# Kernel tuning notes

Hardware: AMD Instinct MI355X
Metric: run time of the kernel (lower is better)

The kernel has to match this reference:

```python
import jax, jax.numpy as jnp
import numpy as np

UNITS = 1024
ORDER = 256
THETA = 512.0
D_IN = 256
BATCH = 64
SEQ = 512


def _legendre_zoh(order, theta):
    """Legendre delay system (Voelker & Eliasmith 2018), ZOH-discretized at dt=1.
    Returns AT = (A_d - I).T and BT = B_d.T, matching LMUCell's stored weights."""
    Q = np.arange(order, dtype=np.float64)
    R = (2.0 * Q + 1.0)[:, None] / theta
    j, i = np.meshgrid(Q, Q)
    A = np.where(i < j, -1.0, (-1.0) ** (i - j + 1)) * R
    B = ((-1.0) ** Q)[:, None] * R
    Aj = jnp.asarray(A, jnp.float32)
    Bj = jnp.asarray(B, jnp.float32)
    Ad = jax.scipy.linalg.expm(Aj)                      # expm(A*dt), dt=1
    Bd = jnp.linalg.solve(Aj, (Ad - jnp.eye(order, dtype=jnp.float32)) @ Bj)
    AT = (Ad - jnp.eye(order, dtype=jnp.float32)).T     # (order, order)
    BT = Bd.T                                           # (1, order)
    return AT, BT


def setup_inputs() -> dict:
    key = jax.random.key(0)
    ks = jax.random.split(key, 6)
    inputs = jax.random.normal(ks[0], (BATCH, SEQ, D_IN), jnp.float32)

    def lecun_uniform(k, fan_in, shape):
        lim = np.sqrt(3.0 / fan_in).astype(np.float32)
        return jax.random.uniform(k, shape, jnp.float32, -lim, lim)

    def glorot_normal(k, fi, fo):
        std = np.sqrt(2.0 / (fi + fo)).astype(np.float32)
        return jax.random.normal(k, (fi, fo), jnp.float32) * std

    input_encoders = lecun_uniform(ks[1], D_IN, (D_IN, 1))
    hidden_encoders = lecun_uniform(ks[2], UNITS, (UNITS, 1))
    memory_encoders = jnp.zeros((ORDER, 1), jnp.float32)  # Constant(0) initializer
    input_kernel = glorot_normal(ks[3], D_IN, UNITS)
    hidden_kernel = glorot_normal(ks[4], UNITS, UNITS)
    memory_kernel = glorot_normal(ks[5], ORDER, UNITS)
    AT, BT = _legendre_zoh(ORDER, THETA)
    return {
        "inputs": inputs,
        "input_encoders": input_encoders,
        "hidden_encoders": hidden_encoders,
        "memory_encoders": memory_encoders,
        "input_kernel": input_kernel,
        "hidden_kernel": hidden_kernel,
        "memory_kernel": memory_kernel,
        "AT": AT,
        "BT": BT,
    }


def reference(inputs, input_encoders, hidden_encoders, memory_encoders,
              input_kernel, hidden_kernel, memory_kernel, AT, BT):
    B = inputs.shape[0]
    order = AT.shape[0]
    units = hidden_kernel.shape[0]
    h0 = jnp.zeros((B, units), inputs.dtype)
    m0 = jnp.zeros((B, order), inputs.dtype)

    def step(carry, x_t):
        h, m = carry
        # u: scalar encoding per batch element, shape [B, 1]
        u = x_t @ input_encoders + h @ hidden_encoders + m @ memory_encoders
        # state-space memory update: m_{t+1} = m + m @ (Ad - I)^T + u @ Bd^T
        m = m + m @ AT + u @ BT
        # hidden update (include_bias=False -> '+ 0')
        h = jnp.tanh(x_t @ input_kernel + h @ hidden_kernel + m @ memory_kernel)
        return (h, m), h

    xs = jnp.swapaxes(inputs, 0, 1)  # [T, B, D]
    (_, _), hs = jax.lax.scan(step, (h0, m0), xs)
    return jnp.swapaxes(hs, 0, 1)    # [B, T, units]
```

## Files before the change

### kernel.cpp

```cpp
#include <hip/hip_runtime.h>
#include <cmath>

static constexpr int UNITS = 1024;
static constexpr int ORDER = 256;
static constexpr int D_IN  = 256;
static constexpr int BATCH = 64;
static constexpr int SEQ   = 512;

static constexpr int GPLANE = 40960;
static constexpr int GSET   = 81920;

static constexpr size_t XE_OFF = 0;
static constexpr size_t FG_OFF = 131072;
static constexpr size_t UP_OFF = 135168;
static constexpr size_t P_OFF  = 176128;
static constexpr size_t PSET   = 327680;

static constexpr int SXH_OFF  = 0;
static constexpr int SXL_OFF  = 8448;
static constexpr int RED_OFF  = 16896;
static constexpr int RED2_OFF = 20992;
static constexpr int ULDS_OFF = 25088;
static constexpr int BVS_OFF  = 25152;
static constexpr int LDS_BYTES = 25216;

typedef __attribute__((ext_vector_type(8))) short bf16x8;
typedef __attribute__((ext_vector_type(4))) float f32x4;
typedef unsigned long long u64;

__device__ __forceinline__ unsigned short bf16rn(float f) {
    unsigned u = __builtin_bit_cast(unsigned, f);
    u += 0x7FFFu + ((u >> 16) & 1u);
    return (unsigned short)(u >> 16);
}
__device__ __forceinline__ float bf2f(unsigned short h) {
    unsigned u = ((unsigned)h) << 16;
    return __builtin_bit_cast(float, u);
}

__device__ __forceinline__ u64 ld_sys(const void* p) {
    return __hip_atomic_load((const u64*)p, __ATOMIC_RELAXED, __HIP_MEMORY_SCOPE_SYSTEM);
}
__device__ __forceinline__ void st_sys32(void* p, unsigned v) {
    __hip_atomic_store((unsigned*)p, v, __ATOMIC_RELAXED, __HIP_MEMORY_SCOPE_SYSTEM);
}
__device__ __forceinline__ bf16x8 mk8(u64 a, u64 b) {
    union { u64 q[2]; bf16x8 v; } u;
    u.q[0] = a; u.q[1] = b;
    return u.v;
}

__global__ __launch_bounds__(256) void lmu_pre(const float* __restrict__ x,
                                               const float* __restrict__ ie,
                                               char* __restrict__ ws) {
    int gid  = blockIdx.x * blockDim.x + threadIdx.x;
    int wave = gid >> 6;
    int lane = gid & 63;
    if (wave < BATCH * SEQ) {
        const float* row = x + (size_t)wave * D_IN;
        float s = 0.f;
        #pragma unroll
        for (int c = 0; c < D_IN; c += 64) s += row[c + lane] * ie[c + lane];
        #pragma unroll
        for (int off = 32; off > 0; off >>= 1) s += __shfl_down(s, off);
        if (lane == 0) ((float*)(ws + XE_OFF))[wave] = s;
    }
    if (gid < 175104) ((unsigned*)(ws + FG_OFF))[gid] = 0u;
}

__global__ __launch_bounds__(256, 1) void lmu_main(
        const float* __restrict__ x,
        const float* __restrict__ he,
        const float* __restrict__ me,
        const float* __restrict__ Wi,
        const float* __restrict__ Wh,
        const float* __restrict__ Wm,
        const float* __restrict__ AT,
        const float* __restrict__ BT,
        float* __restrict__ out,
        char* __restrict__ ws) {
    extern __shared__ char smem[];
    char*  sXH  = smem + SXH_OFF;
    char*  sXL  = smem + SXL_OFF;
    float* REDs = (float*)(smem + RED_OFF);
    float* RED2 = (float*)(smem + RED2_OFF);
    float* ULDS = (float*)(smem + ULDS_OFF);
    float* BVs  = (float*)(smem + BVS_OFF);
    float* WMC  = (float*)smem;

    const int wg = blockIdx.x, tid = threadIdx.x;
    const int wave = tid >> 6, lane = tid & 63;
    const int lrow = lane & 15, lgrp = lane >> 4;
    const int grp = wg >> 6, lid = wg & 63;
    const int b0 = grp * 16, n0 = lid * 16, nglob = n0 + lrow;
    const bool mwg = (lid < 16);
    const int mt = lid & 15;

    float* XE  = (float*)(ws + XE_OFF);
    unsigned* gf = (unsigned*)(ws + FG_OFF) + (size_t)grp * 256;
    float* UPf = (float*)(ws + UP_OFF);
    char* PB   = ws + P_OFF;

    const int lb = (lgrp * 16 + lrow) * 16;

    const int rowME = lgrp * 4 + wave;
    const int kH = 256 + n0 + (lrow & ~1);
    const int hswz = (kH / 32 - 8) * 1024 + (((kH % 32) / 8) * 16 + rowME) * 16
                   + (kH % 8) * 2;
    const int kM = 1280 + mt * 16 + (lrow & ~1);
    const int mswz = (kM / 32 - 8) * 1024 + (((kM % 32) / 8) * 16 + rowME) * 16
                   + (kM % 8) * 2;

    for (int idx = tid; idx < ORDER * 16; idx += 256)
        WMC[idx] = Wm[(size_t)(idx >> 4) * UNITS + n0 + (idx & 15)];
    __syncthreads();

    bf16x8 wfhi[12], wflo[12];
    #pragma unroll
    for (int j = 0; j < 12; ++j) {
        const int kbase = wave * 384 + j * 32 + lgrp * 8;
        bf16x8 vh, vl;
        #pragma unroll
        for (int e = 0; e < 8; ++e) {
            const int k = kbase + e;
            float f;
            if (k < 256)       f = Wi[(size_t)k * UNITS + nglob];
            else if (k < 1280) f = Wh[(size_t)(k - 256) * UNITS + nglob];
            else {
                const int r = k - 1280;
                float s = WMC[r * 16 + lrow];
                const float* atr = AT + (size_t)r * ORDER;
                for (int l = 0; l < ORDER; ++l) s += atr[l] * WMC[l * 16 + lrow];
                f = s;
            }
            unsigned short hb = bf16rn(f);
            unsigned short lb2 = bf16rn(f - bf2f(hb));
            vh[e] = (short)hb; vl[e] = (short)lb2;
        }
        wfhi[j] = vh; wflo[j] = vl;
    }
    {
        const int nl = tid & 15, seg = tid >> 4;
        float s = 0.f;
        for (int l = seg * 16; l < seg * 16 + 16; ++l) s += BT[l] * WMC[l * 16 + nl];
        REDs[tid] = s;
    }
    __syncthreads();
    if (tid < 16) {
        float s = 0.f;
        for (int sg = 0; sg < 16; ++sg) s += REDs[sg * 16 + tid];
        BVs[tid] = s;
    }
    bf16x8 m1hi[2], m1lo[2];
    float btreg = 0.f, mereg = 0.f;
    if (mwg) {
        #pragma unroll
        for (int j2 = 0; j2 < 2; ++j2) {
            const int kb = wave * 64 + j2 * 32 + lgrp * 8;
            const int c = mt * 16 + lrow;
            bf16x8 vh, vl;
            #pragma unroll
            for (int e = 0; e < 8; ++e) {
                const int r = kb + e;
                float f = AT[(size_t)r * ORDER + c] + ((r == c) ? 1.f : 0.f);
                unsigned short hb = bf16rn(f);
                unsigned short lb2 = bf16rn(f - bf2f(hb));
                vh[e] = (short)hb; vl[e] = (short)lb2;
            }
            m1hi[j2] = vh; m1lo[j2] = vl;
        }
        btreg = BT[mt * 16 + lrow];
        mereg = me[mt * 16 + lrow];
    }
    __syncthreads();
    const float bvreg = BVs[lrow];
    const float hereg = he[n0 + lrow];

    for (int t = 0; t < SEQ; ++t) {
        __syncthreads();
        if (tid == 0) {
            asm volatile("s_waitcnt vmcnt(0)\n\t"
                         "global_store_dword %0, %1, off sc0 sc1"
                         :: "v"(gf + lid), "v"((unsigned)(t + 1)) : "memory");
        }

        {
            const int row = tid >> 4, cs = tid & 15;
            const float4* xr = (const float4*)(x + ((size_t)(b0 + row) * SEQ + t) * D_IN
                                               + cs * 16);
            float4 v0 = xr[0], v1 = xr[1], v2 = xr[2], v3 = xr[3];
            float fs[16] = {v0.x,v0.y,v0.z,v0.w, v1.x,v1.y,v1.z,v1.w,
                            v2.x,v2.y,v2.z,v2.w, v3.x,v3.y,v3.z,v3.w};
            unsigned* dh = (unsigned*)(sXH + row * 528 + cs * 32);
            unsigned* dl = (unsigned*)(sXL + row * 528 + cs * 32);
            #pragma unroll
            for (int q = 0; q < 8; ++q) {
                unsigned short h0 = bf16rn(fs[2*q]),   h1 = bf16rn(fs[2*q+1]);
                unsigned short l0 = bf16rn(fs[2*q]   - bf2f(h0));
                unsigned short l1 = bf16rn(fs[2*q+1] - bf2f(h1));
                dh[q] = (unsigned)h0 | ((unsigned)h1 << 16);
                dl[q] = (unsigned)l0 | ((unsigned)l1 << 16);
            }
        }

        if (tid < 64) {
            const unsigned* fp = gf + tid;
            unsigned v;
            const unsigned gen = (unsigned)(t + 1);
            for (;;) {
                asm volatile("global_load_dword %0, %1, off sc0 sc1\n\t"
                             "s_waitcnt vmcnt(0)"
                             : "=v"(v) : "v"(fp) : "memory");
                if (v >= gen) break;
                __builtin_amdgcn_s_sleep(1);
            }
        }
        __syncthreads();
        __builtin_amdgcn_sched_barrier(0);

        const char* GH = PB + (size_t)(t & 1) * PSET + (size_t)grp * GSET;
        const char* GL = GH + GPLANE;

        u64 ah0[12], ah1[12], al0[12], al1[12];
        if (wave == 0) {
            #pragma unroll
            for (int j = 8; j < 12; ++j) {
                const int off = (j - 8) * 1024 + lb;
                ah0[j] = ld_sys(GH + off);     ah1[j] = ld_sys(GH + off + 8);
                al0[j] = ld_sys(GL + off);     al1[j] = ld_sys(GL + off + 8);
            }
        } else {
            #pragma unroll
            for (int j = 0; j < 12; ++j) {
                const int off = (wave * 12 + j - 8) * 1024 + lb;
                ah0[j] = ld_sys(GH + off);     ah1[j] = ld_sys(GH + off + 8);
                al0[j] = ld_sys(GL + off);     al1[j] = ld_sys(GL + off + 8);
            }
        }
        u64 mh0[2], mh1[2], ml0[2], ml1[2];
        if (mwg) {
            #pragma unroll
            for (int j2 = 0; j2 < 2; ++j2) {
                const int off = (32 + 2 * wave + j2) * 1024 + lb;
                mh0[j2] = ld_sys(GH + off);    mh1[j2] = ld_sys(GH + off + 8);
                ml0[j2] = ld_sys(GL + off);    ml1[j2] = ld_sys(GL + off + 8);
            }
        }
        u64 upv[10];
        if (wave == 0) {
            const int bl = lane >> 2, q = lane & 3;
            const char* pp = (const char*)(UPf + ((size_t)(t & 1) * 64 + b0 + bl) * 80
                                           + q * 20);
            #pragma unroll
            for (int i = 0; i < 10; ++i) upv[i] = ld_sys(pp + i * 8);
        }

        f32x4 acc = {0.f, 0.f, 0.f, 0.f};
        if (wave == 0) {
            #pragma unroll
            for (int j = 0; j < 8; ++j) {
                const char* xp = sXH + lrow * 528 + (j * 32 + lgrp * 8) * 2;
                bf16x8 ah = *(const bf16x8*)xp;
                bf16x8 al = *(const bf16x8*)(xp + 8448);
                acc = __builtin_amdgcn_mfma_f32_16x16x32_bf16(ah, wfhi[j], acc, 0, 0, 0);
                acc = __builtin_amdgcn_mfma_f32_16x16x32_bf16(ah, wflo[j], acc, 0, 0, 0);
                acc = __builtin_amdgcn_mfma_f32_16x16x32_bf16(al, wfhi[j], acc, 0, 0, 0);
            }
            #pragma unroll
            for (int j = 8; j < 12; ++j) {
                bf16x8 ah = mk8(ah0[j], ah1[j]);
                bf16x8 al = mk8(al0[j], al1[j]);
                acc = __builtin_amdgcn_mfma_f32_16x16x32_bf16(ah, wfhi[j], acc, 0, 0, 0);
                acc = __builtin_amdgcn_mfma_f32_16x16x32_bf16(ah, wflo[j], acc, 0, 0, 0);
                acc = __builtin_amdgcn_mfma_f32_16x16x32_bf16(al, wfhi[j], acc, 0, 0, 0);
            }
        } else {
            #pragma unroll
            for (int j = 0; j < 12; ++j) {
                bf16x8 ah = mk8(ah0[j], ah1[j]);
                bf16x8 al = mk8(al0[j], al1[j]);
                acc = __builtin_amdgcn_mfma_f32_16x16x32_bf16(ah, wfhi[j], acc, 0, 0, 0);
                acc = __builtin_amdgcn_mfma_f32_16x16x32_bf16(ah, wflo[j], acc, 0, 0, 0);
                acc = __builtin_amdgcn_mfma_f32_16x16x32_bf16(al, wfhi[j], acc, 0, 0, 0);
            }
        }
        f32x4 acc2 = {0.f, 0.f, 0.f, 0.f};
        if (mwg) {
            #pragma unroll
            for (int j2 = 0; j2 < 2; ++j2) {
                bf16x8 ah = mk8(mh0[j2], mh1[j2]);
                bf16x8 al = mk8(ml0[j2], ml1[j2]);
                acc2 = __builtin_amdgcn_mfma_f32_16x16x32_bf16(ah, m1hi[j2], acc2, 0, 0, 0);
                acc2 = __builtin_amdgcn_mfma_f32_16x16x32_bf16(ah, m1lo[j2], acc2, 0, 0, 0);
                acc2 = __builtin_amdgcn_mfma_f32_16x16x32_bf16(al, m1hi[j2], acc2, 0, 0, 0);
            }
        }

        if (wave == 0) {
            const int bl = lane >> 2, q = lane & 3;
            float s = 0.f;
            #pragma unroll
            for (int i = 0; i < 10; ++i) {
                s += __builtin_bit_cast(float, (unsigned)(upv[i] & 0xFFFFFFFFu))
                   + __builtin_bit_cast(float, (unsigned)(upv[i] >> 32));
            }
            s += __shfl_xor(s, 1, 64);
            s += __shfl_xor(s, 2, 64);
            if (q == 0) ULDS[bl] = XE[(size_t)(b0 + bl) * SEQ + t] + s;
        }

        #pragma unroll
        for (int r = 0; r < 4; ++r) {
            REDs[r * 256 + wave * 64 + lane] = acc[r];
            if (mwg) RED2[r * 256 + wave * 64 + lane] = acc2[r];
        }
        __syncthreads();

        {
            const int w = wave;
            const int b = b0 + rowME;
            float a0 = REDs[w * 256 + 0 * 64 + lane] + REDs[w * 256 + 1 * 64 + lane]
                     + REDs[w * 256 + 2 * 64 + lane] + REDs[w * 256 + 3 * 64 + lane];
            const float uu = ULDS[rowME];
            const float hval = tanhf(a0 + uu * bvreg);
            out[((size_t)b * SEQ + t) * UNITS + n0 + lrow] = hval;

            char* PNH = PB + (size_t)((t + 1) & 1) * PSET + (size_t)grp * GSET;
            char* PNL = PNH + GPLANE;
            unsigned hb = bf16rn(hval);
            unsigned lb2 = bf16rn(hval - bf2f((unsigned short)hb));
            unsigned hbn = __shfl_xor(hb, 1, 64);
            unsigned lbn = __shfl_xor(lb2, 1, 64);
            if (!(lrow & 1)) {
                st_sys32(PNH + hswz, hb | (hbn << 16));
                st_sys32(PNL + hswz, lb2 | (lbn << 16));
            }
            float ps = hval * hereg;
            ps += __shfl_xor(ps, 1, 64);
            ps += __shfl_xor(ps, 2, 64);
            ps += __shfl_xor(ps, 4, 64);
            ps += __shfl_xor(ps, 8, 64);
            float* UPn = UPf + (size_t)(((t + 1) & 1) * 64) * 80;
            if (lrow == 0)
                st_sys32(&UPn[(size_t)b * 80 + lid], __builtin_bit_cast(unsigned, ps));
            if (mwg) {
                float a2 = RED2[w * 256 + 0 * 64 + lane] + RED2[w * 256 + 1 * 64 + lane]
                         + RED2[w * 256 + 2 * 64 + lane] + RED2[w * 256 + 3 * 64 + lane];
                const float mval = a2 + uu * btreg;
                unsigned mh = bf16rn(mval);
                unsigned ml = bf16rn(mval - bf2f((unsigned short)mh));
                unsigned mhn = __shfl_xor(mh, 1, 64);
                unsigned mln = __shfl_xor(ml, 1, 64);
                if (!(lrow & 1)) {
                    st_sys32(PNH + mswz, mh | (mhn << 16));
                    st_sys32(PNL + mswz, ml | (mln << 16));
                }
                float pm = mval * mereg;
                pm += __shfl_xor(pm, 1, 64);
                pm += __shfl_xor(pm, 2, 64);
                pm += __shfl_xor(pm, 4, 64);
                pm += __shfl_xor(pm, 8, 64);
                if (lrow == 0)
                    st_sys32(&UPn[(size_t)b * 80 + 64 + mt],
                             __builtin_bit_cast(unsigned, pm));
            }
        }
    }
}

extern "C" void kernel_launch(void* const* d_in, const int* in_sizes, int n_in,
                              void* d_out, int out_size, void* d_ws, size_t ws_size,
                              hipStream_t stream) {
    const float* x  = (const float*)d_in[0];
    const float* ie = (const float*)d_in[1];
    const float* he = (const float*)d_in[2];
    const float* me = (const float*)d_in[3];
    const float* Wi = (const float*)d_in[4];
    const float* Wh = (const float*)d_in[5];
    const float* Wm = (const float*)d_in[6];
    const float* AT = (const float*)d_in[7];
    const float* BT = (const float*)d_in[8];
    float* out = (float*)d_out;
    char* ws   = (char*)d_ws;
    (void)in_sizes; (void)n_in; (void)out_size; (void)ws_size;

    hipLaunchKernelGGL(lmu_pre, dim3((BATCH * SEQ * 64) / 256), dim3(256), 0, stream,
                       x, ie, ws);

    hipLaunchKernelGGL(lmu_main, dim3(256), dim3(256), LDS_BYTES, stream,
                       x, he, me, Wi, Wh, Wm, AT, BT, out, ws);
}
```

Measured before the change: 3.070 ms.

## Balance K split across waves and use per-wave flags for grid barrier

```diff
diff --git a/kernel.cpp b/kernel.cpp
--- a/kernel.cpp
+++ b/kernel.cpp
@@ -118,7 +118,8 @@
     bf16x8 wfhi[12], wflo[12];
     #pragma unroll
     for (int j = 0; j < 12; ++j) {
-        const int kbase = wave * 384 + j * 32 + lgrp * 8;
+        const int cell = (j < 2) ? (2 * wave + j) : (8 + wave * 10 + (j - 2));
+        const int kbase = cell * 32 + lgrp * 8;
         bf16x8 vh, vl;
         #pragma unroll
         for (int e = 0; e < 8; ++e) {
@@ -177,13 +178,6 @@
     const float hereg = he[n0 + lrow];
 
     for (int t = 0; t < SEQ; ++t) {
-        __syncthreads();
-        if (tid == 0) {
-            asm volatile("s_waitcnt vmcnt(0)\n\t"
-                         "global_store_dword %0, %1, off sc0 sc1"
-                         :: "v"(gf + lid), "v"((unsigned)(t + 1)) : "memory");
-        }
-
         {
             const int row = tid >> 4, cs = tid & 15;
             const float4* xr = (const float4*)(x + ((size_t)(b0 + row) * SEQ + t) * D_IN
@@ -203,17 +197,15 @@
             }
         }
 
-        if (tid < 64) {
+        {
+            const unsigned gen = (unsigned)t;
             const unsigned* fp = gf + tid;
             unsigned v;
-            const unsigned gen = (unsigned)(t + 1);
-            for (;;) {
+            do {
                 asm volatile("global_load_dword %0, %1, off sc0 sc1\n\t"
                              "s_waitcnt vmcnt(0)"
                              : "=v"(v) : "v"(fp) : "memory");
-                if (v >= gen) break;
-                __builtin_amdgcn_s_sleep(1);
-            }
+            } while (v < gen);
         }
         __syncthreads();
         __builtin_amdgcn_sched_barrier(0);
@@ -221,21 +213,12 @@
         const char* GH = PB + (size_t)(t & 1) * PSET + (size_t)grp * GSET;
         const char* GL = GH + GPLANE;
 
-        u64 ah0[12], ah1[12], al0[12], al1[12];
-        if (wave == 0) {
-            #pragma unroll
-            for (int j = 8; j < 12; ++j) {
-                const int off = (j - 8) * 1024 + lb;
-                ah0[j] = ld_sys(GH + off);     ah1[j] = ld_sys(GH + off + 8);
-                al0[j] = ld_sys(GL + off);     al1[j] = ld_sys(GL + off + 8);
-            }
-        } else {
-            #pragma unroll
-            for (int j = 0; j < 12; ++j) {
-                const int off = (wave * 12 + j - 8) * 1024 + lb;
-                ah0[j] = ld_sys(GH + off);     ah1[j] = ld_sys(GH + off + 8);
-                al0[j] = ld_sys(GL + off);     al1[j] = ld_sys(GL + off + 8);
-            }
+        u64 ah0[10], ah1[10], al0[10], al1[10];
+        #pragma unroll
+        for (int j2 = 0; j2 < 10; ++j2) {
+            const int off = (wave * 10 + j2) * 1024 + lb;
+            ah0[j2] = ld_sys(GH + off);    ah1[j2] = ld_sys(GH + off + 8);
+            al0[j2] = ld_sys(GL + off);    al1[j2] = ld_sys(GL + off + 8);
         }
         u64 mh0[2], mh1[2], ml0[2], ml1[2];
         if (mwg) {
@@ -256,33 +239,22 @@
         }
 
         f32x4 acc = {0.f, 0.f, 0.f, 0.f};
-        if (wave == 0) {
-            #pragma unroll
-            for (int j = 0; j < 8; ++j) {
-                const char* xp = sXH + lrow * 528 + (j * 32 + lgrp * 8) * 2;
-                bf16x8 ah = *(const bf16x8*)xp;
-                bf16x8 al = *(const bf16x8*)(xp + 8448);
-                acc = __builtin_amdgcn_mfma_f32_16x16x32_bf16(ah, wfhi[j], acc, 0, 0, 0);
-                acc = __builtin_amdgcn_mfma_f32_16x16x32_bf16(ah, wflo[j], acc, 0, 0, 0);
-                acc = __builtin_amdgcn_mfma_f32_16x16x32_bf16(al, wfhi[j], acc, 0, 0, 0);
-            }
-            #pragma unroll
-            for (int j = 8; j < 12; ++j) {
-                bf16x8 ah = mk8(ah0[j], ah1[j]);
-                bf16x8 al = mk8(al0[j], al1[j]);
-                acc = __builtin_amdgcn_mfma_f32_16x16x32_bf16(ah, wfhi[j], acc, 0, 0, 0);
-                acc = __builtin_amdgcn_mfma_f32_16x16x32_bf16(ah, wflo[j], acc, 0, 0, 0);
-                acc = __builtin_amdgcn_mfma_f32_16x16x32_bf16(al, wfhi[j], acc, 0, 0, 0);
-            }
-        } else {
-            #pragma unroll
-            for (int j = 0; j < 12; ++j) {
-                bf16x8 ah = mk8(ah0[j], ah1[j]);
-                bf16x8 al = mk8(al0[j], al1[j]);
-                acc = __builtin_amdgcn_mfma_f32_16x16x32_bf16(ah, wfhi[j], acc, 0, 0, 0);
-                acc = __builtin_amdgcn_mfma_f32_16x16x32_bf16(ah, wflo[j], acc, 0, 0, 0);
-                acc = __builtin_amdgcn_mfma_f32_16x16x32_bf16(al, wfhi[j], acc, 0, 0, 0);
-            }
+        #pragma unroll
+        for (int j = 0; j < 2; ++j) {
+            const char* xp = sXH + lrow * 528 + ((2 * wave + j) * 32 + lgrp * 8) * 2;
+            bf16x8 ah = *(const bf16x8*)xp;
+            bf16x8 al = *(const bf16x8*)(xp + 8448);
+            acc = __builtin_amdgcn_mfma_f32_16x16x32_bf16(ah, wfhi[j], acc, 0, 0, 0);
+            acc = __builtin_amdgcn_mfma_f32_16x16x32_bf16(ah, wflo[j], acc, 0, 0, 0);
+            acc = __builtin_amdgcn_mfma_f32_16x16x32_bf16(al, wfhi[j], acc, 0, 0, 0);
+        }
+        #pragma unroll
+        for (int j2 = 0; j2 < 10; ++j2) {
+            bf16x8 ah = mk8(ah0[j2], ah1[j2]);
+            bf16x8 al = mk8(al0[j2], al1[j2]);
+            acc = __builtin_amdgcn_mfma_f32_16x16x32_bf16(ah, wfhi[2 + j2], acc, 0, 0, 0);
+            acc = __builtin_amdgcn_mfma_f32_16x16x32_bf16(ah, wflo[2 + j2], acc, 0, 0, 0);
+            acc = __builtin_amdgcn_mfma_f32_16x16x32_bf16(al, wfhi[2 + j2], acc, 0, 0, 0);
         }
         f32x4 acc2 = {0.f, 0.f, 0.f, 0.f};
         if (mwg) {
@@ -365,6 +337,13 @@
                              __builtin_bit_cast(unsigned, pm));
             }
         }
+
+        if (lane == 0) {
+            asm volatile("s_waitcnt vmcnt(0)\n\t"
+                         "global_store_dword %0, %1, off sc0 sc1"
+                         :: "v"(gf + lid * 4 + wave), "v"((unsigned)(t + 1))
+                         : "memory");
+        }
     }
 }
 
```

Result: no change. 3.124 ms (+1.8%).
